# Kernel optimization log

Hardware: AMD Instinct MI355X
Metric: run time of the kernel (lower is better)

## Reference

```python
import jax, jax.numpy as jnp
import numpy as np

B, N, F = 8, 1024, 256
H, U = 4, 256
NEG = -1e9  # unused (adjacency=None -> full attention)


def setup_inputs() -> dict:
    key = jax.random.key(0)
    k1, k2, k3, k4 = jax.random.split(key, 4)
    x = jax.random.normal(k1, (B, N, F), dtype=jnp.float32)
    # glorot-scale params
    W = jax.random.normal(k2, (H, F, U), dtype=jnp.float32) * (2.0 / (F + U)) ** 0.5
    a_src = jax.random.normal(k3, (H, U, 1), dtype=jnp.float32) * (2.0 / (U + 1)) ** 0.5
    a_dst = jax.random.normal(k4, (H, U, 1), dtype=jnp.float32) * (2.0 / (U + 1)) ** 0.5
    return {"x": x, "W": W, "a_src": a_src, "a_dst": a_dst}


def reference(x, W, a_src, a_dst):
    # per-head linear projection: [B,H,N,U]
    h = jnp.einsum('bnf,hfu->bhnu', x, W)
    # additive attention logits
    src = jnp.einsum('bhnu,hu->bhn', h, a_src[..., 0])  # [B,H,N]
    dst = jnp.einsum('bhnu,hu->bhn', h, a_dst[..., 0])  # [B,H,N]
    scores = src[:, :, :, None] + dst[:, :, None, :]    # [B,H,N,N]
    scores = jax.nn.leaky_relu(scores, negative_slope=0.2)
    attn = jax.nn.softmax(scores, axis=-1)
    h_prime = jnp.einsum('bhnm,bhmu->bhnu', attn, h)    # [B,H,N,U]
    # concat heads: [B,N,H*U]
    return jnp.transpose(h_prime, (0, 2, 1, 3)).reshape(B, N, H * U)
```

## Files before the change

### kernel.cpp

```cpp
#include <hip/hip_runtime.h>
#include <math.h>

constexpr int B_ = 8, N_ = 1024, F_ = 256, H_ = 4, U_ = 256;
constexpr int BH_ = B_ * H_;
constexpr int CH_ = 16;
constexpr int NCH_ = N_ / CH_;
constexpr int M_ = B_ * N_;

typedef short short8 __attribute__((ext_vector_type(8)));
typedef float floatx4 __attribute__((ext_vector_type(4)));

__device__ inline unsigned short f2bf(float f) {
    unsigned u = __float_as_uint(f);
    u += 0x7fff + ((u >> 16) & 1);
    return (unsigned short)(u >> 16);
}
__device__ inline float bf2f(unsigned short s) { return __uint_as_float(((unsigned)s) << 16); }

__device__ inline void gload_lds16(const void* g, void* l) {
    __builtin_amdgcn_global_load_lds(
        (const __attribute__((address_space(1))) void*)g,
        (__attribute__((address_space(3))) void*)(unsigned)(uintptr_t)l,
        16, 0, 0);
}

__global__ __launch_bounds__(256) void prep_w(const float* __restrict__ W,
                                              const float* __restrict__ asr,
                                              const float* __restrict__ ads,
                                              unsigned short* __restrict__ whT,
                                              float* __restrict__ c_src,
                                              float* __restrict__ c_dst) {
    int tid = threadIdx.x;
    if (blockIdx.x < 64) {
        __shared__ float t[64][65];
        int bi = blockIdx.x;
        int f0 = (bi & 3) * 64, u0 = ((bi >> 2) & 3) * 64, h = bi >> 4;
        int c = tid & 63, rbase = tid >> 6;
        #pragma unroll
        for (int rr = 0; rr < 16; ++rr) {
            int r = rr * 4 + rbase;
            t[r][c] = W[((size_t)(h * F_ + f0 + r)) * U_ + u0 + c];
        }
        __syncthreads();
        #pragma unroll
        for (int rr = 0; rr < 16; ++rr) {
            int r = rr * 4 + rbase;
            whT[((size_t)(h * U_ + u0 + r)) * F_ + f0 + c] = f2bf(t[c][r]);
        }
    } else {
        int id = blockIdx.x - 64;
        int h = id >> 2, f0 = (id & 3) * 64;
        int fl = tid >> 2, q = tid & 3;
        int f = f0 + fl;
        const float* Wrow = W + ((size_t)(h * F_ + f)) * U_ + q * 64;
        const float* av = asr + h * U_ + q * 64;
        const float* bv = ads + h * U_ + q * 64;
        float s = 0.f, d = 0.f;
        #pragma unroll
        for (int u = 0; u < 64; ++u) { float ww = Wrow[u]; s += ww * av[u]; d += ww * bv[u]; }
        s += __shfl_xor(s, 1); s += __shfl_xor(s, 2);
        d += __shfl_xor(d, 1); d += __shfl_xor(d, 2);
        if (q == 0) { c_src[h * F_ + f] = s; c_dst[h * F_ + f] = d; }
    }
}

__global__ __launch_bounds__(256) void k1b_fused(const float* __restrict__ x,
                                                 const float* __restrict__ c_src,
                                                 const float* __restrict__ c_dst,
                                                 unsigned short* __restrict__ xh,
                                                 float* __restrict__ srcv,
                                                 float* __restrict__ dstv) {
    int tid = threadIdx.x;
    int lane = tid & 63, w = tid >> 6;
    int row = blockIdx.x * 4 + w;
    int b = row >> 10, n = row & 1023;
    const float4 x4 = *(const float4*)(x + (size_t)row * F_ + lane * 4);
    ushort4 hv;
    hv.x = f2bf(x4.x); hv.y = f2bf(x4.y); hv.z = f2bf(x4.z); hv.w = f2bf(x4.w);
    ((ushort4*)xh)[(size_t)row * (F_ / 4) + lane] = hv;
    #pragma unroll
    for (int hh = 0; hh < H_; ++hh) {
        float4 c4 = *(const float4*)(c_src + hh * F_ + lane * 4);
        float s = x4.x*c4.x + x4.y*c4.y + x4.z*c4.z + x4.w*c4.w;
        #pragma unroll
        for (int off = 32; off; off >>= 1) s += __shfl_xor(s, off);
        float4 d4 = *(const float4*)(c_dst + hh * F_ + lane * 4);
        float d = x4.x*d4.x + x4.y*d4.y + x4.z*d4.z + x4.w*d4.w;
        #pragma unroll
        for (int off = 32; off; off >>= 1) d += __shfl_xor(d, off);
        if (lane == 0) {
            srcv[(size_t)(b * H_ + hh) * N_ + n] = s;
            dstv[(size_t)(b * H_ + hh) * N_ + n] = d;
        }
    }
}

__global__ __launch_bounds__(1024) void k2_all(const float* __restrict__ dstv,
                                               const float* __restrict__ srcv,
                                               float* __restrict__ dvs,
                                               int* __restrict__ invp,
                                               int* __restrict__ spos,
                                               int* __restrict__ srows,
                                               float* __restrict__ se8,
                                               int* __restrict__ cstart) {
    __shared__ float dv[N_];
    __shared__ float keyLA[N_]; __shared__ int idxLA[N_];
    __shared__ float keyLB[N_]; __shared__ int idxLB[N_];
    int bh = blockIdx.x, t = threadIdx.x;

    float ka = dstv[(size_t)bh * N_ + t];  int ia = t;
    float kb = -srcv[(size_t)bh * N_ + t]; int ib = t;

    for (int k = 2; k <= N_; k <<= 1) {
        for (int j = k >> 1; j > 0; j >>= 1) {
            bool up = ((t & k) == 0);
            bool lower = ((t & j) == 0);
            float oa, ob; int oia, oib;
            if (j >= 64) {
                keyLA[t] = ka; idxLA[t] = ia;
                keyLB[t] = kb; idxLB[t] = ib;
                __syncthreads();
                oa = keyLA[t ^ j]; oia = idxLA[t ^ j];
                ob = keyLB[t ^ j]; oib = idxLB[t ^ j];
                __syncthreads();
            } else {
                oa = __shfl_xor(ka, j); oia = __shfl_xor(ia, j);
                ob = __shfl_xor(kb, j); oib = __shfl_xor(ib, j);
            }
            bool swa = up ? (lower ? (ka > oa) : (ka < oa))
                          : (lower ? (ka < oa) : (ka > oa));
            if (swa) { ka = oa; ia = oia; }
            bool swb = up ? (lower ? (kb > ob) : (kb < ob))
                          : (lower ? (kb < ob) : (kb > ob));
            if (swb) { kb = ob; ib = oib; }
        }
    }

    dvs[(size_t)bh * N_ + t] = ka;
    invp[(size_t)bh * N_ + ia] = t;
    dv[t] = ka;
    __syncthreads();

    float s = -kb;
    int lo = 0, hi = N_;
    while (lo < hi) {
        int mid = (lo + hi) >> 1;
        if (dv[mid] <= kb) lo = mid + 1; else hi = mid;
    }
    spos[(size_t)bh * N_ + t] = lo;
    srows[(size_t)bh * N_ + t] = ib;
    se8[(size_t)bh * N_ + t] = expf(0.8f * s);
    idxLA[t] = lo;
    __syncthreads();
    if (t < NCH_ + 1) {
        int target = t * CH_;
        int lo2 = 0, hi2 = N_;
        while (lo2 < hi2) {
            int mid = (lo2 + hi2) >> 1;
            if (idxLA[mid] < target) lo2 = mid + 1; else hi2 = mid;
        }
        cstart[bh * (NCH_ + 1) + t] = lo2;
    }
}

__global__ __launch_bounds__(256) void k1_mfma(const unsigned short* __restrict__ xh,
                                               const unsigned short* __restrict__ whT,
                                               const int* __restrict__ invp,
                                               unsigned short* __restrict__ hbuf) {
    __shared__ __align__(16) unsigned short As[2 * 128 * 64];
    __shared__ int jsL[128];
    unsigned short* Bs = As + 128 * 64;
    const int tid = threadIdx.x;
    const int lane = tid & 63, wv = tid >> 6;
    const int wr = wv >> 1, wc = wv & 1;
    const int m0 = blockIdx.x * 128;
    const int u0 = blockIdx.y * 128;
    const int hh = blockIdx.z;
    const int b = m0 >> 10, n0 = m0 & 1023;
    const int bh = b * H_ + hh;

    if (tid < 128) jsL[tid] = invp[(size_t)bh * N_ + n0 + tid];

    floatx4 acc[4][4] = {};

    const char* Asrc = (const char*)xh;
    const char* Bsrc = (const char*)(whT + (size_t)hh * U_ * F_);

    const int ch_row = lane >> 3;
    const int ch_col = (lane & 7) * 16;

    for (int t = 0; t < 4; ++t) {
        const size_t kb = (size_t)t * 128;
        #pragma unroll
        for (int i = 0; i < 4; ++i) {
            int c = wv * 4 + i;
            int row = c * 8 + ch_row;
            gload_lds16(Asrc + (size_t)(m0 + row) * 512 + kb + ch_col,
                        (char*)As + c * 1024);
            gload_lds16(Bsrc + (size_t)(u0 + row) * 512 + kb + ch_col,
                        (char*)Bs + c * 1024);
        }
        __syncthreads();
        #pragma unroll
        for (int ks = 0; ks < 2; ++ks) {
            short8 af[4], bfr[4];
            #pragma unroll
            for (int mf = 0; mf < 4; ++mf) {
                int row = wr * 64 + mf * 16 + (lane & 15);
                af[mf] = *(const short8*)&As[row * 64 + ks * 32 + (lane >> 4) * 8];
            }
            #pragma unroll
            for (int nf = 0; nf < 4; ++nf) {
                int row = wc * 64 + nf * 16 + (lane & 15);
                bfr[nf] = *(const short8*)&Bs[row * 64 + ks * 32 + (lane >> 4) * 8];
            }
            #pragma unroll
            for (int mf = 0; mf < 4; ++mf)
                #pragma unroll
                for (int nf = 0; nf < 4; ++nf)
                    acc[mf][nf] = __builtin_amdgcn_mfma_f32_16x16x32_bf16(
                        af[mf], bfr[nf], acc[mf][nf], 0, 0, 0);
        }
        __syncthreads();
    }

    unsigned short* S = As;
    const int rquad = (lane >> 4) * 4;
    const int ucol = lane & 15;
    #pragma unroll
    for (int mf = 0; mf < 4; ++mf)
        #pragma unroll
        for (int j = 0; j < 4; ++j) {
            int rloc = wr * 64 + mf * 16 + rquad + j;
            #pragma unroll
            for (int nf = 0; nf < 4; ++nf)
                S[rloc * 128 + wc * 64 + nf * 16 + ucol] = f2bf(acc[mf][nf][j]);
        }
    __syncthreads();
    #pragma unroll
    for (int i = 0; i < 8; ++i) {
        int flat = tid + i * 256;
        int rloc = flat >> 4, slot = flat & 15;
        short8 v = *(const short8*)&S[rloc * 128 + slot * 8];
        *(short8*)&hbuf[((size_t)bh * N_ + jsL[rloc]) * U_ + u0 + slot * 8] = v;
    }
}

__global__ __launch_bounds__(256) void k3a_partial(const unsigned short* __restrict__ hbuf,
                                                   const float* __restrict__ dvs,
                                                   float* __restrict__ cT1, float* __restrict__ cT2,
                                                   float* __restrict__ cZ1, float* __restrict__ cZ2) {
    __shared__ float w1s[CH_], w2s[CH_];
    __shared__ floatx4 A1s[4][64], A2s[4][64];
    int bh = blockIdx.x / NCH_, c = blockIdx.x % NCH_;
    int tid = threadIdx.x, w = tid >> 6, l = tid & 63;
    const ushort4* hb4 = (const ushort4*)(hbuf + ((size_t)bh * N_ + c * CH_) * U_);
    ushort4 h0 = hb4[(4 * w + 0) * 64 + l];
    ushort4 h1 = hb4[(4 * w + 1) * 64 + l];
    ushort4 h2 = hb4[(4 * w + 2) * 64 + l];
    ushort4 h3 = hb4[(4 * w + 3) * 64 + l];
    floatx4 v0 = {bf2f(h0.x), bf2f(h0.y), bf2f(h0.z), bf2f(h0.w)};
    floatx4 v1 = {bf2f(h1.x), bf2f(h1.y), bf2f(h1.z), bf2f(h1.w)};
    floatx4 v2 = {bf2f(h2.x), bf2f(h2.y), bf2f(h2.z), bf2f(h2.w)};
    floatx4 v3 = {bf2f(h3.x), bf2f(h3.y), bf2f(h3.z), bf2f(h3.w)};
    if (tid < CH_) {
        float vv = dvs[(size_t)bh * N_ + c * CH_ + tid];
        w1s[tid] = expf(vv);
        w2s[tid] = expf(0.2f * vv);
    }
    __syncthreads();
    floatx4 s1 = w1s[4*w]*v0 + w1s[4*w+1]*v1 + w1s[4*w+2]*v2 + w1s[4*w+3]*v3;
    floatx4 s2 = w2s[4*w]*v0 + w2s[4*w+1]*v1 + w2s[4*w+2]*v2 + w2s[4*w+3]*v3;
    A1s[w][l] = s1; A2s[w][l] = s2;
    __syncthreads();
    if (tid < 64) {
        floatx4 r1 = A1s[0][tid] + A1s[1][tid] + A1s[2][tid] + A1s[3][tid];
        floatx4 r2 = A2s[0][tid] + A2s[1][tid] + A2s[2][tid] + A2s[3][tid];
        ((floatx4*)(cT1 + (size_t)(bh * NCH_ + c) * U_))[tid] = r1;
        ((floatx4*)(cT2 + (size_t)(bh * NCH_ + c) * U_))[tid] = r2;
    }
    if (tid == 0) {
        float z1 = 0.f, z2 = 0.f;
        #pragma unroll
        for (int r = 0; r < CH_; ++r) { z1 += w1s[r]; z2 += w2s[r]; }
        cZ1[bh * NCH_ + c] = z1; cZ2[bh * NCH_ + c] = z2;
    }
}

__global__ __launch_bounds__(256) void k3b_combine(const float* __restrict__ cT1, const float* __restrict__ cT2,
                                                   const float* __restrict__ cZ1, const float* __restrict__ cZ2,
                                                   float* __restrict__ b1, float* __restrict__ b2,
                                                   float* __restrict__ bz1, float* __restrict__ bz2) {
    __shared__ float tot1[4][64], tot2[4][64];
    int bh = blockIdx.x >> 2, q = blockIdx.x & 3;
    int l = threadIdx.x & 63, seg = threadIdx.x >> 6;
    int ucol = q * 64 + l;

    float v1[16], v2[16];
    #pragma unroll
    for (int k = 0; k < 16; ++k) {
        int cc = seg * 16 + k;
        v1[k] = cT1[(size_t)(bh * NCH_ + cc) * U_ + ucol];
        v2[k] = cT2[(size_t)(bh * NCH_ + cc) * U_ + ucol];
    }
    float T1 = 0.f, T2 = 0.f;
    #pragma unroll
    for (int k = 0; k < 16; ++k) { T1 += v1[k]; T2 += v2[k]; }
    tot1[seg][l] = T1; tot2[seg][l] = T2;
    __syncthreads();
    float base2 = 0.f, base1 = 0.f;
    #pragma unroll
    for (int ss = 0; ss < 4; ++ss) {
        if (ss < seg) base2 += tot2[ss][l];
        if (ss > seg) base1 += tot1[ss][l];
    }
    float acc2 = base2;
    #pragma unroll
    for (int k = 0; k < 16; ++k) {
        b2[(size_t)(bh * NCH_ + seg * 16 + k) * U_ + ucol] = acc2;
        acc2 += v2[k];
    }
    float acc1 = base1;
    #pragma unroll
    for (int k = 15; k >= 0; --k) {
        b1[(size_t)(bh * NCH_ + seg * 16 + k) * U_ + ucol] = acc1;
        acc1 += v1[k];
    }

    if (q == 0 && threadIdx.x < NCH_) {
        int u = threadIdx.x;
        float z1 = cZ1[bh * NCH_ + u];
        float z2 = cZ2[bh * NCH_ + u];
        float i1 = z1, i2 = z2;
        #pragma unroll
        for (int off = 1; off < NCH_; off <<= 1) {
            float t1 = __shfl_up(i1, off, 64);
            float t2 = __shfl_up(i2, off, 64);
            if (u >= off) { i1 += t1; i2 += t2; }
        }
        float tot = __shfl(i1, NCH_ - 1, 64);
        bz1[bh * NCH_ + u] = tot - i1;
        bz2[bh * NCH_ + u] = i2 - z2;
    }
}

__global__ __launch_bounds__(256) void k3cd_emit(const unsigned short* __restrict__ hbuf,
                                                 const float* __restrict__ dvs,
                                                 const float* __restrict__ b1, const float* __restrict__ b2,
                                                 const float* __restrict__ bz1, const float* __restrict__ bz2,
                                                 const int* __restrict__ spos,
                                                 const int* __restrict__ srows,
                                                 const float* __restrict__ se8,
                                                 const int* __restrict__ cstart,
                                                 float* __restrict__ out) {
    __shared__ floatx4 P1s[CH_ + 1][64];
    __shared__ floatx4 P2s[CH_ + 1][64];
    __shared__ floatx4 T1s[4][64], T2s[4][64];
    __shared__ float w1s[CH_], w2s[CH_];
    __shared__ float zx1[CH_ + 1], zx2[CH_ + 1];
    __shared__ int sps[256], srs[256];
    __shared__ float s8s[256];

    int bh = blockIdx.x / NCH_, c = blockIdx.x % NCH_;
    int tid = threadIdx.x, w = tid >> 6, l = tid & 63;
    int b = bh >> 2, hh = bh & 3;

    const int*   spos_b  = spos  + (size_t)bh * N_;
    const int*   srows_b = srows + (size_t)bh * N_;
    const float* se8_b   = se8   + (size_t)bh * N_;
    const int j0 = cstart[bh * (NCH_ + 1) + c];
    const int e0 = (c == NCH_ - 1) ? N_ : cstart[bh * (NCH_ + 1) + c + 1];
    int sp0 = 0, sr0 = 0; float s80 = 0.f;
    {
        int jj = j0 + tid;
        if (jj < e0) { sp0 = spos_b[jj]; sr0 = srows_b[jj]; s80 = se8_b[jj]; }
    }
    floatx4 b1u = ((const floatx4*)(b1 + (size_t)(bh * NCH_ + c) * U_))[l];
    floatx4 b2u = ((const floatx4*)(b2 + (size_t)(bh * NCH_ + c) * U_))[l];
    float bz1c = bz1[bh * NCH_ + c], bz2c = bz2[bh * NCH_ + c];

    const ushort4* hb4 = (const ushort4*)(hbuf + ((size_t)bh * N_ + c * CH_) * U_);
    ushort4 h0 = hb4[(4 * w + 0) * 64 + l];
    ushort4 h1 = hb4[(4 * w + 1) * 64 + l];
    ushort4 h2 = hb4[(4 * w + 2) * 64 + l];
    ushort4 h3 = hb4[(4 * w + 3) * 64 + l];
    floatx4 v0 = {bf2f(h0.x), bf2f(h0.y), bf2f(h0.z), bf2f(h0.w)};
    floatx4 v1 = {bf2f(h1.x), bf2f(h1.y), bf2f(h1.z), bf2f(h1.w)};
    floatx4 v2 = {bf2f(h2.x), bf2f(h2.y), bf2f(h2.z), bf2f(h2.w)};
    floatx4 v3 = {bf2f(h3.x), bf2f(h3.y), bf2f(h3.z), bf2f(h3.w)};
    if (tid < CH_) {
        float vv = dvs[(size_t)bh * N_ + c * CH_ + tid];
        w1s[tid] = expf(vv);
        w2s[tid] = expf(0.2f * vv);
    }
    __syncthreads();
    float a0 = w1s[4*w], a1 = w1s[4*w+1], a2 = w1s[4*w+2], a3 = w1s[4*w+3];
    float c0 = w2s[4*w], c1 = w2s[4*w+1], c2 = w2s[4*w+2], c3 = w2s[4*w+3];
    floatx4 q1_1 = a0 * v0;
    floatx4 q1_2 = q1_1 + a1 * v1;
    floatx4 q1_3 = q1_2 + a2 * v2;
    floatx4 tw1  = q1_3 + a3 * v3;
    floatx4 q2_1 = c0 * v0;
    floatx4 q2_2 = q2_1 + c1 * v1;
    floatx4 q2_3 = q2_2 + c2 * v2;
    floatx4 tw2  = q2_3 + c3 * v3;
    T1s[w][l] = tw1; T2s[w][l] = tw2;
    if (tid == 0) {
        float z1 = 0.f, z2 = 0.f;
        #pragma unroll
        for (int r = 0; r < CH_; ++r) { zx1[r] = z1; zx2[r] = z2; z1 += w1s[r]; z2 += w2s[r]; }
        zx1[CH_] = z1; zx2[CH_] = z2;
    }
    __syncthreads();
    floatx4 base1 = {0.f, 0.f, 0.f, 0.f}, base2 = {0.f, 0.f, 0.f, 0.f};
    if (w > 0) { base1 += T1s[0][l]; base2 += T2s[0][l]; }
    if (w > 1) { base1 += T1s[1][l]; base2 += T2s[1][l]; }
    if (w > 2) { base1 += T1s[2][l]; base2 += T2s[2][l]; }
    P1s[4*w+0][l] = base1;         P2s[4*w+0][l] = base2;
    P1s[4*w+1][l] = base1 + q1_1;  P2s[4*w+1][l] = base2 + q2_1;
    P1s[4*w+2][l] = base1 + q1_2;  P2s[4*w+2][l] = base2 + q2_2;
    P1s[4*w+3][l] = base1 + q1_3;  P2s[4*w+3][l] = base2 + q2_3;
    if (w == 3) { P1s[CH_][l] = base1 + tw1; P2s[CH_][l] = base2 + tw2; }
    __syncthreads();

    floatx4 t1 = P1s[CH_][l];
    float tz1 = zx1[CH_];

    for (int t0 = j0; t0 < e0; t0 += 256) {
        if (t0 == j0) {
            sps[tid] = sp0; srs[tid] = sr0; s8s[tid] = s80;
        } else {
            int jj = t0 + tid;
            if (jj < e0) { sps[tid] = spos_b[jj]; srs[tid] = srows_b[jj]; s8s[tid] = se8_b[jj]; }
        }
        __syncthreads();
        int cnt = min(256, e0 - t0);
        for (int k = w; k < cnt; k += 4) {
            int   rr  = sps[k] - c * CH_;
            int   row = srs[k];
            float e8  = s8s[k];
            floatx4 s1 = b1u + (t1 - P1s[rr][l]);
            floatx4 s2 = b2u + P2s[rr][l];
            float den = e8 * (bz1c + (tz1 - zx1[rr])) + (bz2c + zx2[rr]);
            float rden = 1.0f / den;
            floatx4 o = (e8 * s1 + s2) * rden;
            __builtin_nontemporal_store(o,
                (floatx4*)(out + ((size_t)(b * N_ + row)) * (H_ * U_) + hh * U_ + 4 * l));
        }
        __syncthreads();
    }
}

extern "C" void kernel_launch(void* const* d_in, const int* in_sizes, int n_in,
                              void* d_out, int out_size, void* d_ws, size_t ws_size,
                              hipStream_t stream) {
    const float* x    = (const float*)d_in[0];
    const float* W    = (const float*)d_in[1];
    const float* asr  = (const float*)d_in[2];
    const float* ads  = (const float*)d_in[3];
    float* out = (float*)d_out;

    char* ws = (char*)d_ws;
    size_t off = 0;
    auto alloc = [&](size_t nfloats) -> float* {
        float* p = (float*)(ws + off);
        off += ((nfloats * 4 + 255) / 256) * 256;
        return p;
    };
    unsigned short* hbuf = (unsigned short*)alloc((size_t)BH_ * N_ * U_ / 2);
    float* srcv  = alloc((size_t)BH_ * N_);
    float* dstv  = alloc((size_t)BH_ * N_);
    float* c_src = alloc(H_ * F_);
    float* c_dst = alloc(H_ * F_);
    float* dvs   = alloc((size_t)BH_ * N_);
    int*   invp  = (int*)alloc((size_t)BH_ * N_);
    int*   srows = (int*)alloc((size_t)BH_ * N_);
    int*   spos  = (int*)alloc((size_t)BH_ * N_);
    float* se8   = alloc((size_t)BH_ * N_);
    int*   cstart= (int*)alloc(BH_ * (NCH_ + 1));
    float* cT1   = alloc((size_t)BH_ * NCH_ * U_);
    float* cT2   = alloc((size_t)BH_ * NCH_ * U_);
    float* cZ1   = alloc(BH_ * NCH_);
    float* cZ2   = alloc(BH_ * NCH_);
    float* b1    = alloc((size_t)BH_ * NCH_ * U_);
    float* b2    = alloc((size_t)BH_ * NCH_ * U_);
    float* bz1   = alloc(BH_ * NCH_);
    float* bz2   = alloc(BH_ * NCH_);
    unsigned short* xh  = (unsigned short*)alloc((size_t)M_ * F_ / 2);
    unsigned short* whT = (unsigned short*)alloc((size_t)H_ * U_ * F_ / 2);
    (void)ws_size; (void)in_sizes; (void)n_in; (void)out_size;

    prep_w<<<80, 256, 0, stream>>>(W, asr, ads, whT, c_src, c_dst);
    k1b_fused<<<(B_ * N_) / 4, 256, 0, stream>>>(x, c_src, c_dst, xh, srcv, dstv);
    k2_all<<<BH_, 1024, 0, stream>>>(dstv, srcv, dvs, invp, spos, srows, se8, cstart);
    k1_mfma<<<dim3(M_ / 128, U_ / 128, H_), 256, 0, stream>>>(xh, whT, invp, hbuf);
    k3a_partial<<<BH_ * NCH_, 256, 0, stream>>>(hbuf, dvs, cT1, cT2, cZ1, cZ2);
    k3b_combine<<<BH_ * 4, 256, 0, stream>>>(cT1, cT2, cZ1, cZ2, b1, b2, bz1, bz2);
    k3cd_emit<<<BH_ * NCH_, 256, 0, stream>>>(hbuf, dvs, b1, b2, bz1, bz2,
                                              spos, srows, se8, cstart, out);
}
```

Before: 79.81 us.

## Fuse chunk-combine scan into partial kernel via last-block atomic counter

Removes the separate k3b_combine launch. Each k3a_partial block now increments a per-(batch,head) atomic counter, and the last block to finish for that head computes the prefix and suffix scans over the chunk partials and the Z totals. This saves one kernel launch and its dependency gap. In exchange, the combine work for each head runs serially in a single block over all four column quarters, and a memset is added to reset the counters before the kernels run.

After: 318.0 us. 3.98x slower.

```diff
diff --git a/kernel.cpp b/kernel.cpp
--- a/kernel.cpp
+++ b/kernel.cpp
@@ -249,9 +249,13 @@
 __global__ __launch_bounds__(256) void k3a_partial(const unsigned short* __restrict__ hbuf,
                                                    const float* __restrict__ dvs,
                                                    float* __restrict__ cT1, float* __restrict__ cT2,
-                                                   float* __restrict__ cZ1, float* __restrict__ cZ2) {
+                                                   float* __restrict__ cZ1, float* __restrict__ cZ2,
+                                                   float* __restrict__ b1, float* __restrict__ b2,
+                                                   float* __restrict__ bz1, float* __restrict__ bz2,
+                                                   int* __restrict__ cnt) {
     __shared__ float w1s[CH_], w2s[CH_];
     __shared__ floatx4 A1s[4][64], A2s[4][64];
+    __shared__ int amLast;
     int bh = blockIdx.x / NCH_, c = blockIdx.x % NCH_;
     int tid = threadIdx.x, w = tid >> 6, l = tid & 63;
     const ushort4* hb4 = (const ushort4*)(hbuf + ((size_t)bh * N_ + c * CH_) * U_);
@@ -285,50 +289,53 @@
         for (int r = 0; r < CH_; ++r) { z1 += w1s[r]; z2 += w2s[r]; }
         cZ1[bh * NCH_ + c] = z1; cZ2[bh * NCH_ + c] = z2;
     }
-}
-
-__global__ __launch_bounds__(256) void k3b_combine(const float* __restrict__ cT1, const float* __restrict__ cT2,
-                                                   const float* __restrict__ cZ1, const float* __restrict__ cZ2,
-                                                   float* __restrict__ b1, float* __restrict__ b2,
-                                                   float* __restrict__ bz1, float* __restrict__ bz2) {
-    __shared__ float tot1[4][64], tot2[4][64];
-    int bh = blockIdx.x >> 2, q = blockIdx.x & 3;
-    int l = threadIdx.x & 63, seg = threadIdx.x >> 6;
-    int ucol = q * 64 + l;
-
-    float v1[16], v2[16];
+
+    __threadfence();
+    if (tid == 0) amLast = (atomicAdd(&cnt[bh], 1) == NCH_ - 1) ? 1 : 0;
+    __syncthreads();
+    if (!amLast) return;
+    __threadfence();
+
+    __shared__ float tt1[4][64], tt2[4][64];
+    const int seg = w;
     #pragma unroll
-    for (int k = 0; k < 16; ++k) {
-        int cc = seg * 16 + k;
-        v1[k] = cT1[(size_t)(bh * NCH_ + cc) * U_ + ucol];
-        v2[k] = cT2[(size_t)(bh * NCH_ + cc) * U_ + ucol];
-    }
-    float T1 = 0.f, T2 = 0.f;
-    #pragma unroll
-    for (int k = 0; k < 16; ++k) { T1 += v1[k]; T2 += v2[k]; }
-    tot1[seg][l] = T1; tot2[seg][l] = T2;
-    __syncthreads();
-    float base2 = 0.f, base1 = 0.f;
-    #pragma unroll
-    for (int ss = 0; ss < 4; ++ss) {
-        if (ss < seg) base2 += tot2[ss][l];
-        if (ss > seg) base1 += tot1[ss][l];
-    }
-    float acc2 = base2;
-    #pragma unroll
-    for (int k = 0; k < 16; ++k) {
-        b2[(size_t)(bh * NCH_ + seg * 16 + k) * U_ + ucol] = acc2;
-        acc2 += v2[k];
-    }
-    float acc1 = base1;
-    #pragma unroll
-    for (int k = 15; k >= 0; --k) {
-        b1[(size_t)(bh * NCH_ + seg * 16 + k) * U_ + ucol] = acc1;
-        acc1 += v1[k];
-    }
-
-    if (q == 0 && threadIdx.x < NCH_) {
-        int u = threadIdx.x;
+    for (int q = 0; q < 4; ++q) {
+        int ucol = q * 64 + l;
+        float v1r[16], v2r[16];
+        #pragma unroll
+        for (int k = 0; k < 16; ++k) {
+            int cc = seg * 16 + k;
+            v1r[k] = cT1[(size_t)(bh * NCH_ + cc) * U_ + ucol];
+            v2r[k] = cT2[(size_t)(bh * NCH_ + cc) * U_ + ucol];
+        }
+        float T1 = 0.f, T2 = 0.f;
+        #pragma unroll
+        for (int k = 0; k < 16; ++k) { T1 += v1r[k]; T2 += v2r[k]; }
+        tt1[seg][l] = T1; tt2[seg][l] = T2;
+        __syncthreads();
+        float base2 = 0.f, base1 = 0.f;
+        #pragma unroll
+        for (int ss = 0; ss < 4; ++ss) {
+            if (ss < seg) base2 += tt2[ss][l];
+            if (ss > seg) base1 += tt1[ss][l];
+        }
+        float acc2 = base2;
+        #pragma unroll
+        for (int k = 0; k < 16; ++k) {
+            b2[(size_t)(bh * NCH_ + seg * 16 + k) * U_ + ucol] = acc2;
+            acc2 += v2r[k];
+        }
+        float acc1 = base1;
+        #pragma unroll
+        for (int k = 15; k >= 0; --k) {
+            b1[(size_t)(bh * NCH_ + seg * 16 + k) * U_ + ucol] = acc1;
+            acc1 += v1r[k];
+        }
+        __syncthreads();
+    }
+
+    if (tid < NCH_) {
+        int u = tid;
         float z1 = cZ1[bh * NCH_ + u];
         float z2 = cZ2[bh * NCH_ + u];
         float i1 = z1, i2 = z2;
@@ -434,8 +441,8 @@
             if (jj < e0) { sps[tid] = spos_b[jj]; srs[tid] = srows_b[jj]; s8s[tid] = se8_b[jj]; }
         }
         __syncthreads();
-        int cnt = min(256, e0 - t0);
-        for (int k = w; k < cnt; k += 4) {
+        int cnt2 = min(256, e0 - t0);
+        for (int k = w; k < cnt2; k += 4) {
             int   rr  = sps[k] - c * CH_;
             int   row = srs[k];
             float e8  = s8s[k];
@@ -486,16 +493,18 @@
     float* b2    = alloc((size_t)BH_ * NCH_ * U_);
     float* bz1   = alloc(BH_ * NCH_);
     float* bz2   = alloc(BH_ * NCH_);
+    int*   cnt   = (int*)alloc(BH_);
     unsigned short* xh  = (unsigned short*)alloc((size_t)M_ * F_ / 2);
     unsigned short* whT = (unsigned short*)alloc((size_t)H_ * U_ * F_ / 2);
     (void)ws_size; (void)in_sizes; (void)n_in; (void)out_size;
 
+    hipMemsetAsync(cnt, 0, BH_ * sizeof(int), stream);
     prep_w<<<80, 256, 0, stream>>>(W, asr, ads, whT, c_src, c_dst);
     k1b_fused<<<(B_ * N_) / 4, 256, 0, stream>>>(x, c_src, c_dst, xh, srcv, dstv);
     k2_all<<<BH_, 1024, 0, stream>>>(dstv, srcv, dvs, invp, spos, srows, se8, cstart);
     k1_mfma<<<dim3(M_ / 128, U_ / 128, H_), 256, 0, stream>>>(xh, whT, invp, hbuf);
-    k3a_partial<<<BH_ * NCH_, 256, 0, stream>>>(hbuf, dvs, cT1, cT2, cZ1, cZ2);
-    k3b_combine<<<BH_ * 4, 256, 0, stream>>>(cT1, cT2, cZ1, cZ2, b1, b2, bz1, bz2);
+    k3a_partial<<<BH_ * NCH_, 256, 0, stream>>>(hbuf, dvs, cT1, cT2, cZ1, cZ2,
+                                                b1, b2, bz1, bz2, cnt);
     k3cd_emit<<<BH_ * NCH_, 256, 0, stream>>>(hbuf, dvs, b1, b2, bz1, bz2,
                                               spos, srows, se8, cstart, out);
 }
```
